# Kernel optimization log

Measured on AMD Instinct MI355X. Metric: run time of the kernel, lower is better.

The kernel has to match this reference:

```python
import jax, jax.numpy as jnp
import numpy as np
import math

D_MODEL = 1024
HEAD_DIM = 256
GAMMA = 0.9


def setup_inputs() -> dict:
    key = jax.random.key(0)
    k1, k2, k3, k4 = jax.random.split(key, 4)
    B, L = 4, 4096
    x = jax.random.normal(k1, (B, L, D_MODEL), dtype=jnp.float32)
    s = 1.0 / math.sqrt(D_MODEL)
    W_Q = jax.random.normal(k2, (HEAD_DIM, D_MODEL), dtype=jnp.float32) * s
    W_K = jax.random.normal(k3, (HEAD_DIM, D_MODEL), dtype=jnp.float32) * s
    W_V = jax.random.normal(k4, (HEAD_DIM, D_MODEL), dtype=jnp.float32) * s
    return {"x": x, "W_Q": W_Q, "W_K": W_K, "W_V": W_V}


def _decay_mask(L: int, gamma: float) -> jnp.ndarray:
    # D[i,j] = gamma^(i-j) if i >= j else 0
    idx = jnp.arange(L)
    diff = idx[:, None] - idx[None, :]
    return jnp.where(diff >= 0, jnp.power(jnp.float32(gamma), diff.astype(jnp.float32)), 0.0)


def reference(x, W_Q, W_K, W_V):
    B, L, _ = x.shape
    Q = jnp.einsum('bld,hd->blh', x, W_Q)  # (B,L,H)
    K = jnp.einsum('bld,hd->blh', x, W_K)
    V = jnp.einsum('bld,hd->blh', x, W_V)
    D = _decay_mask(L, GAMMA)  # (L,L)
    scores = jnp.einsum('bih,bjh->bij', Q, K) * D[None, :, :]
    scores = scores / jnp.sqrt(jnp.float32(HEAD_DIM))
    return jnp.einsum('bij,bjh->bih', scores, V)  # (B,L,H)
```

## Files before the change

### kernel.cpp

```cpp
#include <hip/hip_runtime.h>

typedef unsigned short u16;
typedef unsigned int u32;
typedef __attribute__((ext_vector_type(8))) short bf16x8;
typedef __attribute__((ext_vector_type(4))) float f32x4;
typedef __attribute__((ext_vector_type(4))) unsigned short u16x4;

#define DEVI __device__ __forceinline__
#define AS1 __attribute__((address_space(1)))
#define AS3 __attribute__((address_space(3)))

constexpr float L2GAMMA = -0.15200309344504997f;
constexpr float INV_SQRT_H = 0.0625f;

DEVI u16 f2bf(float x) {
  union { float f; unsigned u; } v; v.f = x;
  unsigned r = v.u + 0x7FFFu + ((v.u >> 16) & 1u);
  return (u16)(r >> 16);
}

DEVI u32 pack2bf(float f0, float f1) {
  u32 u0 = __float_as_uint(f0) + 0x8000u;
  u32 u1 = __float_as_uint(f1) + 0x8000u;
  return __builtin_amdgcn_perm(u1, u0, 0x07060302u);
}

__global__ void cvt_w_kernel(const float4* __restrict__ wq, const float4* __restrict__ wk,
                             const float4* __restrict__ wv, u16x4* __restrict__ dst) {
  int i = blockIdx.x * blockDim.x + threadIdx.x;
  int w = i >> 16, off = i & 65535;
  const float4* s = (w == 0) ? wq : ((w == 1) ? wk : wv);
  float4 v = s[off];
  u16x4 o; o.x = f2bf(v.x); o.y = f2bf(v.y); o.z = f2bf(v.z); o.w = f2bf(v.w);
  dst[(w << 16) + off] = o;
}

__global__ __launch_bounds__(256, 3) void qkv_gemm_kernel(const float* __restrict__ Xf, const u16* __restrict__ Wb,
                                                          u16* __restrict__ Qb, u16* __restrict__ Kb,
                                                          u16* __restrict__ Vt) {
  __shared__ float Af[128 * 32];
  __shared__ u16 Bl[128 * 32];
  const int lin = blockIdx.x;
  const int rl = (lin & 7) * 96 + (lin >> 3);
  const int nt = rl % 6;
  const int m0 = (rl / 6) * 128;
  const int n0 = nt * 128;
  const int tid = threadIdx.x;
  const int wid = tid >> 6, lane = tid & 63;
  const int wm = wid >> 1, wn = wid & 1;
  const int lrow = lane & 15, lkg = lane >> 4;
  const int arow_in = lane >> 3;
  const int aslot_src = (lane & 7) ^ arow_in;
  const int brow_in = lane >> 2;
  const int bslot_src = (lane & 3) ^ ((lane >> 3) & 3);

  f32x4 acc[4][4] = {};

  for (int kt = 0; kt < 32; ++kt) {
    const int k0 = kt * 32;
#pragma unroll
    for (int r = 0; r < 4; ++r) {
      const int c = wid * 4 + r;
      const float* g = Xf + (size_t)(m0 + c * 8 + arow_in) * 1024 + k0 + aslot_src * 4;
      __builtin_amdgcn_global_load_lds((const AS1 void*)g, (AS3 void*)&Af[c * 256], 16, 0, 0);
    }
#pragma unroll
    for (int r = 0; r < 2; ++r) {
      const int c = wid * 2 + r;
      const u16* g = Wb + (size_t)(n0 + c * 16 + brow_in) * 1024 + k0 + bslot_src * 8;
      __builtin_amdgcn_global_load_lds((const AS1 void*)g, (AS3 void*)&Bl[c * 512], 16, 0, 0);
    }
    __syncthreads();
    bf16x8 a[4], b[4];
#pragma unroll
    for (int mf = 0; mf < 4; ++mf) {
      const int row = wm * 64 + mf * 16 + lrow;
      const int e0 = (2 * lkg) ^ (lrow & 7);
      const float4 lo = *(const float4*)&Af[row * 32 + e0 * 4];
      const float4 hi = *(const float4*)&Af[row * 32 + (e0 ^ 1) * 4];
      union { u32 w[4]; bf16x8 v; } ua;
      ua.w[0] = pack2bf(lo.x, lo.y); ua.w[1] = pack2bf(lo.z, lo.w);
      ua.w[2] = pack2bf(hi.x, hi.y); ua.w[3] = pack2bf(hi.z, hi.w);
      a[mf] = ua.v;
    }
#pragma unroll
    for (int nf = 0; nf < 4; ++nf) {
      const int row = wn * 64 + nf * 16 + lrow;
      const int s = lkg ^ ((row >> 1) & 3);
      b[nf] = *(const bf16x8*)&Bl[row * 32 + s * 8];
    }
#pragma unroll
    for (int mf = 0; mf < 4; ++mf)
#pragma unroll
      for (int nf = 0; nf < 4; ++nf)
        acc[mf][nf] = __builtin_amdgcn_mfma_f32_16x16x32_bf16(a[mf], b[nf], acc[mf][nf], 0, 0, 0);
    __syncthreads();
  }

  const int rbase = lkg * 4;
  if (nt < 4) {
    u16* Dst = (nt < 2) ? Qb : Kb;
    const int cb = (nt < 2) ? n0 : (n0 - 256);
#pragma unroll
    for (int mf = 0; mf < 4; ++mf)
#pragma unroll
      for (int nf = 0; nf < 4; ++nf) {
        const int gm = m0 + wm * 64 + mf * 16 + rbase;
        const int c = cb + wn * 64 + nf * 16 + lrow;
#pragma unroll
        for (int r = 0; r < 4; ++r) Dst[(size_t)(gm + r) * 256 + c] = f2bf(acc[mf][nf][r]);
      }
  } else {
#pragma unroll
    for (int mf = 0; mf < 4; ++mf)
#pragma unroll
      for (int nf = 0; nf < 4; ++nf) {
        const int gm = m0 + wm * 64 + mf * 16 + rbase;
        const int h = n0 - 512 + wn * 64 + nf * 16 + lrow;
        const int bb = gm >> 12, l = gm & 4095;
        u16x4 pk;
        pk.x = f2bf(acc[mf][nf][0]); pk.y = f2bf(acc[mf][nf][1]);
        pk.z = f2bf(acc[mf][nf][2]); pk.w = f2bf(acc[mf][nf][3]);
        *(u16x4*)&Vt[((size_t)bb * 256 + h) * 4096 + l] = pk;
      }
  }
}

__global__ __launch_bounds__(256) void attn_kernel(const u16* __restrict__ Qb, const u16* __restrict__ Kb,
                                                   const u16* __restrict__ Vt, float* __restrict__ out) {
  __shared__ u16 Plds[32 * 72];
  const int raw = blockIdx.x;
  const int aid = (raw & 7) * 64 + (raw >> 3);
  const int b = aid >> 7;
  const int qt = aid & 127;
  const int qb = qt * 32;
  const int tid = threadIdx.x;
  const int wid = tid >> 6, lane = tid & 63;
  const int lrow = lane & 15, lkg = lane >> 4, lk = lkg * 8;
  const size_t bQK = (size_t)b * 4096 * 256;

  bf16x8 qf[2][8];
#pragma unroll
  for (int mf = 0; mf < 2; ++mf) {
    const u16* Qrow = Qb + bQK + (size_t)(qb + mf * 16 + lrow) * 256;
#pragma unroll
    for (int kf = 0; kf < 8; ++kf) qf[mf][kf] = *(const bf16x8*)&Qrow[kf * 32 + lk];
  }

  int kstart = qb - 256; if (kstart < 0) kstart = 0; kstart &= ~63;
  const int njt = (qb + 32 - kstart + 63) >> 6;

  f32x4 oacc[2][4] = {};

  for (int jt = 0; jt < njt; ++jt) {
    const int kb = kstart + jt * 64;
    f32x4 s[2] = {};
    const u16* Krow = Kb + bQK + (size_t)(kb + wid * 16 + lrow) * 256;
#pragma unroll
    for (int kf = 0; kf < 8; ++kf) {
      const bf16x8 kfr = *(const bf16x8*)&Krow[kf * 32 + lk];
      s[0] = __builtin_amdgcn_mfma_f32_16x16x32_bf16(qf[0][kf], kfr, s[0], 0, 0, 0);
      s[1] = __builtin_amdgcn_mfma_f32_16x16x32_bf16(qf[1][kf], kfr, s[1], 0, 0, 0);
    }
    const int kg = kb + wid * 16 + lrow;
#pragma unroll
    for (int mf = 0; mf < 2; ++mf) {
      const int qg = qb + mf * 16 + lkg * 4;
#pragma unroll
      for (int r = 0; r < 4; ++r) {
        const int d = qg + r - kg;
        const float pv = (d >= 0) ? s[mf][r] * exp2f((float)d * L2GAMMA) * INV_SQRT_H : 0.0f;
        Plds[(mf * 16 + lkg * 4 + r) * 72 + wid * 16 + lrow] = f2bf(pv);
      }
    }
    __syncthreads();
#pragma unroll
    for (int ks = 0; ks < 2; ++ks) {
      bf16x8 pa[2];
      pa[0] = *(const bf16x8*)&Plds[(lrow) * 72 + ks * 32 + lk];
      pa[1] = *(const bf16x8*)&Plds[(16 + lrow) * 72 + ks * 32 + lk];
#pragma unroll
      for (int nf = 0; nf < 4; ++nf) {
        const bf16x8 vb = *(const bf16x8*)&Vt[((size_t)b * 256 + wid * 64 + nf * 16 + lrow) * 4096 + kb + ks * 32 + lk];
        oacc[0][nf] = __builtin_amdgcn_mfma_f32_16x16x32_bf16(pa[0], vb, oacc[0][nf], 0, 0, 0);
        oacc[1][nf] = __builtin_amdgcn_mfma_f32_16x16x32_bf16(pa[1], vb, oacc[1][nf], 0, 0, 0);
      }
    }
    __syncthreads();
  }

#pragma unroll
  for (int mf = 0; mf < 2; ++mf) {
    float* obase = out + ((size_t)b * 4096 + qb + mf * 16 + lkg * 4) * 256 + wid * 64 + lrow;
#pragma unroll
    for (int nf = 0; nf < 4; ++nf)
#pragma unroll
      for (int r = 0; r < 4; ++r)
        obase[(size_t)r * 256 + nf * 16] = oacc[mf][nf][r];
  }
}

extern "C" void kernel_launch(void* const* d_in, const int* in_sizes, int n_in,
                              void* d_out, int out_size, void* d_ws, size_t ws_size,
                              hipStream_t stream) {
  const float* x  = (const float*)d_in[0];
  const float* wq = (const float*)d_in[1];
  const float* wk = (const float*)d_in[2];
  const float* wv = (const float*)d_in[3];
  float* out = (float*)d_out;
  char* ws = (char*)d_ws;
  u16* Wb = (u16*)(ws);
  u16* Qb = (u16*)(ws + (size_t)1572864);
  u16* Kb = (u16*)(ws + (size_t)9961472);
  u16* Vt = (u16*)(ws + (size_t)18350080);

  hipLaunchKernelGGL(cvt_w_kernel, dim3(768), dim3(256), 0, stream,
                     (const float4*)wq, (const float4*)wk, (const float4*)wv, (u16x4*)Wb);
  hipLaunchKernelGGL(qkv_gemm_kernel, dim3(768), dim3(256), 0, stream, x, Wb, Qb, Kb, Vt);
  hipLaunchKernelGGL(attn_kernel, dim3(512), dim3(256), 0, stream, Qb, Kb, Vt, out);
}
```

Before: 76.61 us.

## Register-prefetch GEMM tiles, convert X to bf16 before LDS, pad LDS rows

```diff
diff --git a/kernel.cpp b/kernel.cpp
--- a/kernel.cpp
+++ b/kernel.cpp
@@ -7,8 +7,6 @@
 typedef __attribute__((ext_vector_type(4))) unsigned short u16x4;
 
 #define DEVI __device__ __forceinline__
-#define AS1 __attribute__((address_space(1)))
-#define AS3 __attribute__((address_space(3)))
 
 constexpr float L2GAMMA = -0.15200309344504997f;
 constexpr float INV_SQRT_H = 0.0625f;
@@ -38,8 +36,8 @@
 __global__ __launch_bounds__(256, 3) void qkv_gemm_kernel(const float* __restrict__ Xf, const u16* __restrict__ Wb,
                                                           u16* __restrict__ Qb, u16* __restrict__ Kb,
                                                           u16* __restrict__ Vt) {
-  __shared__ float Af[128 * 32];
-  __shared__ u16 Bl[128 * 32];
+  __shared__ u16 Asw[128 * 40];
+  __shared__ u16 Bsw[128 * 40];
   const int lin = blockIdx.x;
   const int rl = (lin & 7) * 96 + (lin >> 3);
   const int nt = rl % 6;
@@ -49,52 +47,64 @@
   const int wid = tid >> 6, lane = tid & 63;
   const int wm = wid >> 1, wn = wid & 1;
   const int lrow = lane & 15, lkg = lane >> 4;
-  const int arow_in = lane >> 3;
-  const int aslot_src = (lane & 7) ^ arow_in;
-  const int brow_in = lane >> 2;
-  const int bslot_src = (lane & 3) ^ ((lane >> 3) & 3);
+
+  const int a_row = tid >> 3, a_slot = tid & 7;
+  const float* a_g = Xf + (size_t)(m0 + a_row) * 1024 + a_slot * 4;
+  const int a_w = a_row * 40 + a_slot * 4;
+  const int b_row = tid >> 2, b_slot = tid & 3;
+  const u16* b_g = Wb + (size_t)(n0 + b_row) * 1024 + b_slot * 8;
+  const int b_w = b_row * 40 + b_slot * 8;
+
+  float4 arg[4];
+  uint4 brg[2];
+
+#define GISSUE(T) do { \
+  _Pragma("unroll") for (int r_ = 0; r_ < 4; ++r_) \
+    arg[r_] = *(const float4*)(a_g + (size_t)r_ * 32 * 1024 + (T) * 32); \
+  _Pragma("unroll") for (int r_ = 0; r_ < 2; ++r_) \
+    brg[r_] = *(const uint4*)(const void*)(b_g + (size_t)r_ * 64 * 1024 + (T) * 32); \
+} while (0)
+
+#define SWRITE() do { \
+  _Pragma("unroll") for (int r_ = 0; r_ < 4; ++r_) { \
+    uint2 pk_; pk_.x = pack2bf(arg[r_].x, arg[r_].y); pk_.y = pack2bf(arg[r_].z, arg[r_].w); \
+    *(uint2*)&Asw[r_ * 32 * 40 + a_w] = pk_; } \
+  _Pragma("unroll") for (int r_ = 0; r_ < 2; ++r_) \
+    *(uint4*)&Bsw[r_ * 64 * 40 + b_w] = brg[r_]; \
+} while (0)
 
   f32x4 acc[4][4] = {};
 
+  GISSUE(0);
+  SWRITE();
+  asm volatile("s_waitcnt lgkmcnt(0)" ::: "memory");
+  __builtin_amdgcn_s_barrier();
+  __builtin_amdgcn_sched_barrier(0);
+
   for (int kt = 0; kt < 32; ++kt) {
-    const int k0 = kt * 32;
-#pragma unroll
-    for (int r = 0; r < 4; ++r) {
-      const int c = wid * 4 + r;
-      const float* g = Xf + (size_t)(m0 + c * 8 + arow_in) * 1024 + k0 + aslot_src * 4;
-      __builtin_amdgcn_global_load_lds((const AS1 void*)g, (AS3 void*)&Af[c * 256], 16, 0, 0);
-    }
-#pragma unroll
-    for (int r = 0; r < 2; ++r) {
-      const int c = wid * 2 + r;
-      const u16* g = Wb + (size_t)(n0 + c * 16 + brow_in) * 1024 + k0 + bslot_src * 8;
-      __builtin_amdgcn_global_load_lds((const AS1 void*)g, (AS3 void*)&Bl[c * 512], 16, 0, 0);
-    }
-    __syncthreads();
+    if (kt < 31) GISSUE(kt + 1);
+    __builtin_amdgcn_sched_barrier(0);
     bf16x8 a[4], b[4];
 #pragma unroll
-    for (int mf = 0; mf < 4; ++mf) {
-      const int row = wm * 64 + mf * 16 + lrow;
-      const int e0 = (2 * lkg) ^ (lrow & 7);
-      const float4 lo = *(const float4*)&Af[row * 32 + e0 * 4];
-      const float4 hi = *(const float4*)&Af[row * 32 + (e0 ^ 1) * 4];
-      union { u32 w[4]; bf16x8 v; } ua;
-      ua.w[0] = pack2bf(lo.x, lo.y); ua.w[1] = pack2bf(lo.z, lo.w);
-      ua.w[2] = pack2bf(hi.x, hi.y); ua.w[3] = pack2bf(hi.z, hi.w);
-      a[mf] = ua.v;
-    }
-#pragma unroll
-    for (int nf = 0; nf < 4; ++nf) {
-      const int row = wn * 64 + nf * 16 + lrow;
-      const int s = lkg ^ ((row >> 1) & 3);
-      b[nf] = *(const bf16x8*)&Bl[row * 32 + s * 8];
-    }
+    for (int mf = 0; mf < 4; ++mf) a[mf] = *(const bf16x8*)&Asw[(wm * 64 + mf * 16 + lrow) * 40 + lkg * 8];
+#pragma unroll
+    for (int nf = 0; nf < 4; ++nf) b[nf] = *(const bf16x8*)&Bsw[(wn * 64 + nf * 16 + lrow) * 40 + lkg * 8];
+    __builtin_amdgcn_s_setprio(1);
 #pragma unroll
     for (int mf = 0; mf < 4; ++mf)
 #pragma unroll
       for (int nf = 0; nf < 4; ++nf)
         acc[mf][nf] = __builtin_amdgcn_mfma_f32_16x16x32_bf16(a[mf], b[nf], acc[mf][nf], 0, 0, 0);
-    __syncthreads();
+    __builtin_amdgcn_s_setprio(0);
+    asm volatile("s_waitcnt lgkmcnt(0)" ::: "memory");
+    __builtin_amdgcn_s_barrier();
+    __builtin_amdgcn_sched_barrier(0);
+    if (kt < 31) {
+      SWRITE();
+      asm volatile("s_waitcnt lgkmcnt(0)" ::: "memory");
+      __builtin_amdgcn_s_barrier();
+      __builtin_amdgcn_sched_barrier(0);
+    }
   }
 
   const int rbase = lkg * 4;
```

Result: no change. 76.65 us (+0.0%).
